# Kernel optimization log

Measured on AMD Instinct MI355X. Metric: run time of the kernel, lower is better.

## Reference

```python
import jax, jax.numpy as jnp
import numpy as np

N = 8192
IN_F = 512
OUT_F = 512

def setup_inputs() -> dict:
    key = jax.random.key(0)
    k1, k2, k3, k4 = jax.random.split(key, 4)
    input = jax.random.normal(k1, (N, IN_F), dtype=jnp.float32)
    adj = jax.random.uniform(k2, (N, N), dtype=jnp.float32)
    # nn.Linear params: W [out, in], b [out] (kaiming-like scale)
    W = jax.random.normal(k3, (OUT_F, IN_F), dtype=jnp.float32) / np.sqrt(IN_F)
    b = jax.random.normal(k4, (OUT_F,), dtype=jnp.float32) * 0.01
    return {"input": input, "adj": adj, "W": W, "b": b}

def reference(input, adj, W, b):
    # h = Linear(input) = input @ W^T + b   -> [N, OUT_F]
    h = jnp.einsum('ni,oi->no', input, W) + b
    # aggregate over adjacency: adj @ h     -> [N, OUT_F]
    return adj @ h
```

## Files before the change

### kernel.cpp

```cpp
#include <hip/hip_runtime.h>
#include <hip/hip_bf16.h>
#include <stdint.h>

#define NROWS 8192
#define KDIM  512
#define NOUT  512
#define KADJ  8192

using bf16x8   = __attribute__((ext_vector_type(8))) __bf16;
using f32x4    = __attribute__((ext_vector_type(4))) float;
using short4_t = __attribute__((ext_vector_type(4))) short;

__device__ __forceinline__ short f2bf(float f) {
    return (short)__bfloat16_as_ushort(__float2bfloat16(f));
}

__device__ __forceinline__ void gld_lds16(const void* g, void* l) {
    __builtin_amdgcn_global_load_lds(
        (const __attribute__((address_space(1))) void*)g,
        (__attribute__((address_space(3))) void*)l, 16, 0, 0);
}

__global__ __launch_bounds__(256)
void linear_ht_kernel(const float* __restrict__ input,
                      const float* __restrict__ W,
                      const float* __restrict__ bias,
                      short* __restrict__ ht)
{
    __shared__ short Ws[64 * 64];
    __shared__ short Is[128 * 64];

    const int bid  = blockIdx.x;
    const int nblk = bid & 7;
    const int mblk = bid >> 3;
    const int tid  = threadIdx.x;
    const int w    = tid >> 6;
    const int l    = tid & 63;
    const int wm   = w;
    const int lr   = l >> 4, lc = l & 15;

    f32x4 acc[4][2];
    #pragma unroll
    for (int a = 0; a < 4; ++a)
        #pragma unroll
        for (int c = 0; c < 2; ++c) acc[a][c] = (f32x4){0.f, 0.f, 0.f, 0.f};

    const int srow = tid >> 4;
    const int scw  = (tid & 15) * 4;
    const int swz  = (srow & 7) << 4;

    for (int kt = 0; kt < KDIM / 64; ++kt) {
        const int k0 = kt * 64;
        #pragma unroll
        for (int i = 0; i < 4; ++i) {
            int r = srow + i * 16;
            float4 v = *reinterpret_cast<const float4*>(
                W + (size_t)(nblk * 64 + r) * KDIM + k0 + scw);
            short4_t s4 = { f2bf(v.x), f2bf(v.y), f2bf(v.z), f2bf(v.w) };
            int off = r * 128 + ((scw * 2) ^ swz);
            *reinterpret_cast<short4_t*>((char*)Ws + off) = s4;
        }
        #pragma unroll
        for (int i = 0; i < 8; ++i) {
            int r = srow + i * 16;
            float4 v = *reinterpret_cast<const float4*>(
                input + (size_t)(mblk * 128 + r) * KDIM + k0 + scw);
            short4_t s4 = { f2bf(v.x), f2bf(v.y), f2bf(v.z), f2bf(v.w) };
            int off = r * 128 + ((scw * 2) ^ swz);
            *reinterpret_cast<short4_t*>((char*)Is + off) = s4;
        }
        __syncthreads();
        const int kq = lr * 8;
        #pragma unroll
        for (int kk = 0; kk < 2; ++kk) {
            const int lbk = (kk * 32 + kq) * 2;
            bf16x8 af[4], bfr[2];
            #pragma unroll
            for (int fm = 0; fm < 4; ++fm) {
                int r = fm * 16 + lc;
                af[fm] = *reinterpret_cast<const bf16x8*>(
                    (char*)Ws + r * 128 + (lbk ^ ((r & 7) << 4)));
            }
            #pragma unroll
            for (int fb = 0; fb < 2; ++fb) {
                int r = wm * 32 + fb * 16 + lc;
                bfr[fb] = *reinterpret_cast<const bf16x8*>(
                    (char*)Is + r * 128 + (lbk ^ ((r & 7) << 4)));
            }
            #pragma unroll
            for (int fm = 0; fm < 4; ++fm)
                #pragma unroll
                for (int fb = 0; fb < 2; ++fb)
                    acc[fm][fb] = __builtin_amdgcn_mfma_f32_16x16x32_bf16(
                        af[fm], bfr[fb], acc[fm][fb], 0, 0, 0);
        }
        __syncthreads();
    }
    #pragma unroll
    for (int fm = 0; fm < 4; ++fm)
        #pragma unroll
        for (int fb = 0; fb < 2; ++fb)
            #pragma unroll
            for (int j = 0; j < 4; ++j) {
                int n = nblk * 64 + fm * 16 + lr * 4 + j;
                int m = mblk * 128 + wm * 32 + fb * 16 + lc;
                ht[(size_t)n * NROWS + m] = f2bf(acc[fm][fb][j] + bias[n]);
            }
}

__global__ __launch_bounds__(256)
void agg_kernel(const float* __restrict__ adj,
                const short* __restrict__ ht,
                float* __restrict__ out)
{
    __shared__ short As[128 * 64];
    __shared__ short Bs[128 * 64];

    const int bid  = blockIdx.x;
    const int kc   = bid >> 8;
    const int rem  = bid & 255;
    const int brow = rem >> 2;
    const int bcol = rem & 3;
    const int tid  = threadIdx.x;
    const int w    = tid >> 6;
    const int l    = tid & 63;
    const int wr   = w >> 1, wc = w & 1;
    const int lr   = l >> 4, lc = l & 15;

    f32x4 acc[4][4];
    #pragma unroll
    for (int a = 0; a < 4; ++a)
        #pragma unroll
        for (int c = 0; c < 4; ++c) acc[a][c] = (f32x4){0.f, 0.f, 0.f, 0.f};

    const int srow = tid >> 4;
    const int scw  = (tid & 15) * 4;
    const int swz  = (srow & 7) << 4;

    const int br_off = l >> 3;
    const int bcl    = ((l & 7) ^ ((l >> 3) & 7)) * 8;

    for (int kt = 0; kt < 64; ++kt) {
        const int k0 = kc * 4096 + kt * 64;
        #pragma unroll
        for (int i = 0; i < 8; ++i) {
            int r = srow + i * 16;
            float4 v = *reinterpret_cast<const float4*>(
                adj + (size_t)(brow * 128 + r) * KADJ + k0 + scw);
            short4_t s4 = { f2bf(v.x), f2bf(v.y), f2bf(v.z), f2bf(v.w) };
            int off = r * 128 + ((scw * 2) ^ swz);
            *reinterpret_cast<short4_t*>((char*)As + off) = s4;
        }
        #pragma unroll
        for (int j = 0; j < 4; ++j) {
            int s = w * 4 + j;
            int r = s * 8 + br_off;
            gld_lds16(ht + (size_t)(bcol * 128 + r) * KADJ + k0 + bcl,
                      (char*)Bs + s * 1024);
        }
        __syncthreads();
        const int kq = lr * 8;
        #pragma unroll
        for (int kk = 0; kk < 2; ++kk) {
            const int lbk = (kk * 32 + kq) * 2;
            bf16x8 af[4], bfr[4];
            #pragma unroll
            for (int fm = 0; fm < 4; ++fm) {
                int r = wr * 64 + fm * 16 + lc;
                af[fm] = *reinterpret_cast<const bf16x8*>(
                    (char*)As + r * 128 + (lbk ^ ((r & 7) << 4)));
            }
            #pragma unroll
            for (int fn = 0; fn < 4; ++fn) {
                int r = wc * 64 + fn * 16 + lc;
                bfr[fn] = *reinterpret_cast<const bf16x8*>(
                    (char*)Bs + r * 128 + (lbk ^ ((r & 7) << 4)));
            }
            #pragma unroll
            for (int fm = 0; fm < 4; ++fm)
                #pragma unroll
                for (int fn = 0; fn < 4; ++fn)
                    acc[fm][fn] = __builtin_amdgcn_mfma_f32_16x16x32_bf16(
                        af[fm], bfr[fn], acc[fm][fn], 0, 0, 0);
        }
        __syncthreads();
    }
    #pragma unroll
    for (int fm = 0; fm < 4; ++fm)
        #pragma unroll
        for (int fn = 0; fn < 4; ++fn) {
            int row0 = brow * 128 + wr * 64 + fm * 16 + lr * 4;
            int col  = bcol * 128 + wc * 64 + fn * 16 + lc;
            #pragma unroll
            for (int j = 0; j < 4; ++j)
                atomicAdd(&out[(size_t)(row0 + j) * NOUT + col], acc[fm][fn][j]);
        }
}

extern "C" void kernel_launch(void* const* d_in, const int* in_sizes, int n_in,
                              void* d_out, int out_size, void* d_ws, size_t ws_size,
                              hipStream_t stream) {
    const float* input = (const float*)d_in[0];
    const float* adj   = (const float*)d_in[1];
    const float* W     = (const float*)d_in[2];
    const float* bias  = (const float*)d_in[3];
    float* out = (float*)d_out;
    short* ht  = (short*)d_ws;

    hipMemsetAsync(d_out, 0, (size_t)out_size * sizeof(float), stream);

    linear_ht_kernel<<<512, 256, 0, stream>>>(input, W, bias, ht);
    agg_kernel<<<512, 256, 0, stream>>>(adj, ht, out);
}
```

Measured before the change: 493.7 us.

## Double-buffer aggregation GEMM tiles and remap blocks for XCD locality

The aggregation kernel now uses double-buffered LDS for both the adjacency and ht tiles. The next tile's adjacency loads are prefetched into registers and its ht tiles go straight to LDS while MFMA runs on the current buffer, which removes one barrier per iteration. The block index is also remapped so that blocks on the same XCD share the adjacency row tiles, aiming for better L2 reuse of adj across the four column blocks. This doubles LDS use to 64 KB and adds 8 float4 registers per thread, which may lower occupancy.

```diff
diff --git a/kernel.cpp b/kernel.cpp
--- a/kernel.cpp
+++ b/kernel.cpp
@@ -6,6 +6,7 @@
 #define KDIM  512
 #define NOUT  512
 #define KADJ  8192
+#define NT    64
 
 using bf16x8   = __attribute__((ext_vector_type(8))) __bf16;
 using f32x4    = __attribute__((ext_vector_type(4))) float;
@@ -57,8 +58,7 @@
             float4 v = *reinterpret_cast<const float4*>(
                 W + (size_t)(nblk * 64 + r) * KDIM + k0 + scw);
             short4_t s4 = { f2bf(v.x), f2bf(v.y), f2bf(v.z), f2bf(v.w) };
-            int off = r * 128 + ((scw * 2) ^ swz);
-            *reinterpret_cast<short4_t*>((char*)Ws + off) = s4;
+            *reinterpret_cast<short4_t*>((char*)Ws + r * 128 + ((scw * 2) ^ swz)) = s4;
         }
         #pragma unroll
         for (int i = 0; i < 8; ++i) {
@@ -66,8 +66,7 @@
             float4 v = *reinterpret_cast<const float4*>(
                 input + (size_t)(mblk * 128 + r) * KDIM + k0 + scw);
             short4_t s4 = { f2bf(v.x), f2bf(v.y), f2bf(v.z), f2bf(v.w) };
-            int off = r * 128 + ((scw * 2) ^ swz);
-            *reinterpret_cast<short4_t*>((char*)Is + off) = s4;
+            *reinterpret_cast<short4_t*>((char*)Is + r * 128 + ((scw * 2) ^ swz)) = s4;
         }
         __syncthreads();
         const int kq = lr * 8;
@@ -113,14 +112,17 @@
                 const short* __restrict__ ht,
                 float* __restrict__ out)
 {
-    __shared__ short As[128 * 64];
-    __shared__ short Bs[128 * 64];
-
-    const int bid  = blockIdx.x;
-    const int kc   = bid >> 8;
-    const int rem  = bid & 255;
-    const int brow = rem >> 2;
-    const int bcol = rem & 3;
+    __shared__ short As[2][128 * 64];
+    __shared__ short Bs[2][128 * 64];
+
+    const int hw   = blockIdx.x;
+    const int xcd  = hw & 7;
+    const int g    = hw >> 3;
+    const int bcol = g & 3;
+    const int tile = xcd * 16 + (g >> 2);
+    const int brow = tile & 63;
+    const int kc   = tile >> 6;
+
     const int tid  = threadIdx.x;
     const int w    = tid >> 6;
     const int l    = tid & 63;
@@ -136,55 +138,85 @@
     const int srow = tid >> 4;
     const int scw  = (tid & 15) * 4;
     const int swz  = (srow & 7) << 4;
-
-    const int br_off = l >> 3;
-    const int bcl    = ((l & 7) ^ ((l >> 3) & 7)) * 8;
-
-    for (int kt = 0; kt < 64; ++kt) {
-        const int k0 = kc * 4096 + kt * 64;
-        #pragma unroll
-        for (int i = 0; i < 8; ++i) {
-            int r = srow + i * 16;
-            float4 v = *reinterpret_cast<const float4*>(
-                adj + (size_t)(brow * 128 + r) * KADJ + k0 + scw);
-            short4_t s4 = { f2bf(v.x), f2bf(v.y), f2bf(v.z), f2bf(v.w) };
-            int off = r * 128 + ((scw * 2) ^ swz);
-            *reinterpret_cast<short4_t*>((char*)As + off) = s4;
-        }
-        #pragma unroll
-        for (int j = 0; j < 4; ++j) {
-            int s = w * 4 + j;
-            int r = s * 8 + br_off;
-            gld_lds16(ht + (size_t)(bcol * 128 + r) * KADJ + k0 + bcl,
-                      (char*)Bs + s * 1024);
-        }
+    const int bcl  = ((l & 7) ^ ((l >> 3) & 7)) * 8;
+
+    const int    k_base   = kc * 4096;
+    const float* adj_base = adj + (size_t)(brow * 128) * KADJ + k_base;
+    const short* ht_base  = ht + (size_t)(bcol * 128) * KADJ + k_base;
+
+    float4 apf[8];
+
+    #define ISSUE_A(KT)                                                        \
+        _Pragma("unroll")                                                      \
+        for (int i = 0; i < 8; ++i) {                                          \
+            int r = srow + i * 16;                                             \
+            apf[i] = *reinterpret_cast<const float4*>(                         \
+                adj_base + (size_t)r * KADJ + (KT) * 64 + scw);                \
+        }
+
+    #define ISSUE_B(KT, BUF)                                                   \
+        _Pragma("unroll")                                                      \
+        for (int j = 0; j < 4; ++j) {                                          \
+            int s = w * 4 + j;                                                 \
+            int r = s * 8 + (l >> 3);                                          \
+            gld_lds16(ht_base + (size_t)r * KADJ + (KT) * 64 + bcl,            \
+                      (char*)Bs[BUF] + s * 1024);                              \
+        }
+
+    #define WRITE_A(BUF)                                                       \
+        _Pragma("unroll")                                                      \
+        for (int i = 0; i < 8; ++i) {                                          \
+            int r = srow + i * 16;                                             \
+            short4_t s4 = { f2bf(apf[i].x), f2bf(apf[i].y),                    \
+                            f2bf(apf[i].z), f2bf(apf[i].w) };                  \
+            *reinterpret_cast<short4_t*>(                                      \
+                (char*)As[BUF] + r * 128 + ((scw * 2) ^ swz)) = s4;            \
+        }
+
+    #define COMPUTE(BUF)                                                       \
+        {                                                                      \
+            const int kq = lr * 8;                                             \
+            _Pragma("unroll")                                                  \
+            for (int kk = 0; kk < 2; ++kk) {                                   \
+                const int lbk = (kk * 32 + kq) * 2;                            \
+                bf16x8 af[4], bfr[4];                                          \
+                _Pragma("unroll")                                              \
+                for (int fm = 0; fm < 4; ++fm) {                               \
+                    int r = wr * 64 + fm * 16 + lc;                            \
+                    af[fm] = *reinterpret_cast<const bf16x8*>(                 \
+                        (char*)As[BUF] + r * 128 + (lbk ^ ((r & 7) << 4)));    \
+                }                                                              \
+                _Pragma("unroll")                                              \
+                for (int fn = 0; fn < 4; ++fn) {                               \
+                    int r = wc * 64 + fn * 16 + lc;                            \
+                    bfr[fn] = *reinterpret_cast<const bf16x8*>(                \
+                        (char*)Bs[BUF] + r * 128 + (lbk ^ ((r & 7) << 4)));    \
+                }                                                              \
+                _Pragma("unroll")                                              \
+                for (int fm = 0; fm < 4; ++fm)                                 \
+                    _Pragma("unroll")                                          \
+                    for (int fn = 0; fn < 4; ++fn)                             \
+                        acc[fm][fn] = __builtin_amdgcn_mfma_f32_16x16x32_bf16( \
+                            af[fm], bfr[fn], acc[fm][fn], 0, 0, 0);            \
+            }                                                                  \
+        }
+
+    ISSUE_A(0);
+    ISSUE_B(0, 0);
+    WRITE_A(0);
+    __syncthreads();
+
+    int cur = 0;
+    for (int kt = 0; kt < NT - 1; ++kt) {
+        ISSUE_A(kt + 1);
+        ISSUE_B(kt + 1, cur ^ 1);
+        COMPUTE(cur);
+        WRITE_A(cur ^ 1);
         __syncthreads();
-        const int kq = lr * 8;
-        #pragma unroll
-        for (int kk = 0; kk < 2; ++kk) {
-            const int lbk = (kk * 32 + kq) * 2;
-            bf16x8 af[4], bfr[4];
-            #pragma unroll
-            for (int fm = 0; fm < 4; ++fm) {
-                int r = wr * 64 + fm * 16 + lc;
-                af[fm] = *reinterpret_cast<const bf16x8*>(
-                    (char*)As + r * 128 + (lbk ^ ((r & 7) << 4)));
-            }
-            #pragma unroll
-            for (int fn = 0; fn < 4; ++fn) {
-                int r = wc * 64 + fn * 16 + lc;
-                bfr[fn] = *reinterpret_cast<const bf16x8*>(
-                    (char*)Bs + r * 128 + (lbk ^ ((r & 7) << 4)));
-            }
-            #pragma unroll
-            for (int fm = 0; fm < 4; ++fm)
-                #pragma unroll
-                for (int fn = 0; fn < 4; ++fn)
-                    acc[fm][fn] = __builtin_amdgcn_mfma_f32_16x16x32_bf16(
-                        af[fm], bfr[fn], acc[fm][fn], 0, 0, 0);
-        }
-        __syncthreads();
+        cur ^= 1;
     }
+    COMPUTE(cur);
+
     #pragma unroll
     for (int fm = 0; fm < 4; ++fm)
         #pragma unroll
@@ -195,6 +227,11 @@
             for (int j = 0; j < 4; ++j)
                 atomicAdd(&out[(size_t)(row0 + j) * NOUT + col], acc[fm][fn][j]);
         }
+
+    #undef ISSUE_A
+    #undef ISSUE_B
+    #undef WRITE_A
+    #undef COMPUTE
 }
 
 extern "C" void kernel_launch(void* const* d_in, const int* in_sizes, int n_in,
```

After: 552.2 us. 1.12x slower.
